# Kernel optimization log

Hardware: AMD Instinct MI355X
Metric: run time of the kernel (lower is better)

## Reference

```python
import jax, jax.numpy as jnp
import numpy as np

N_NODES = 65536
DEGREE = 16
N_EDGES = N_NODES * DEGREE
IN_CH = 128
HEADS = 4
OUT_CH = 16
NEG_SLOPE = 0.2


def setup_inputs() -> dict:
    key = jax.random.key(0)
    k1, k2, k3, k4, k5, k6 = jax.random.split(key, 6)
    csr_row_ptr = jnp.arange(N_NODES + 1, dtype=jnp.int64) * DEGREE
    csr_col_ind = jax.random.randint(k1, (N_EDGES,), 0, N_NODES, dtype=jnp.int64)
    sample_count = jnp.ones((N_NODES,), dtype=jnp.int64)
    x_neighboor = jax.random.normal(k2, (N_NODES, IN_CH), dtype=jnp.float32)
    x_target = jax.random.normal(k3, (N_NODES, IN_CH), dtype=jnp.float32)
    # xavier-ish init scales
    W = jax.random.normal(k4, (IN_CH, HEADS * OUT_CH), dtype=jnp.float32) * (2.0 / (IN_CH + HEADS * OUT_CH)) ** 0.5
    attn_l = jax.random.normal(k5, (HEADS, OUT_CH), dtype=jnp.float32) * 0.1
    attn_r = jax.random.normal(k6, (HEADS, OUT_CH), dtype=jnp.float32) * 0.1
    bias = jnp.zeros((HEADS * OUT_CH,), dtype=jnp.float32)
    return {"csr_row_ptr": csr_row_ptr, "csr_col_ind": csr_col_ind,
            "sample_count": sample_count, "x_neighboor": x_neighboor,
            "x_target": x_target, "W": W, "attn_l": attn_l,
            "attn_r": attn_r, "bias": bias}


def reference(csr_row_ptr, csr_col_ind, sample_count, x_neighboor, x_target, W, attn_l, attn_r, bias):
    N = csr_row_ptr.shape[0] - 1
    E = csr_col_ind.shape[0]
    H, C = attn_l.shape
    # linear projection: [Nn, in] @ [in, H*C] -> [Nn, H, C]
    feat = (x_neighboor @ W).reshape(-1, H, C)
    feat_target = feat[:N]
    el = jnp.sum(feat_target * attn_l[None], axis=-1)  # [N, H]
    er = jnp.sum(feat * attn_r[None], axis=-1)         # [Nn, H]
    # row id of each edge from CSR row pointers
    row_id = jnp.searchsorted(csr_row_ptr, jnp.arange(E), side='right') - 1  # [E]
    # spadd_gat: per-edge score = el[row] + er[col], then leaky relu
    w = el[row_id] + er[csr_col_ind]                   # [E, H]
    w = jnp.where(w >= 0, w, NEG_SLOPE * w)
    # segment (per-row) softmax over edges, numerically stable
    wmax = jax.lax.stop_gradient(jax.ops.segment_max(w, row_id, num_segments=N))
    ew = jnp.exp(w - wmax[row_id])
    denom = jax.ops.segment_sum(ew, row_id, num_segments=N)
    alpha = ew / denom[row_id]                         # [E, H]
    # weighted sparse aggregation (gspmm): y[r] = sum_e alpha[e] * feat[col[e]]
    y = jax.ops.segment_sum(alpha[:, :, None] * feat[csr_col_ind], row_id, num_segments=N)  # [N, H, C]
    y = y + bias.reshape(1, H, C)
    return y.reshape(N, H * C)
```

## Files before the change

kernel.cpp:

```cpp
#include <hip/hip_runtime.h>
#include <hip/hip_bf16.h>

#define IN_CH 128
#define HC 64
#define NEG_SLOPE 0.2f

typedef __attribute__((ext_vector_type(8))) short short8;
typedef __attribute__((ext_vector_type(4))) float floatx4;

__device__ __forceinline__ unsigned short f2bf_rne(float f) {
    unsigned int u = __float_as_uint(f);
    u += 0x7fffu + ((u >> 16) & 1u);
    return (unsigned short)(u >> 16);
}
__device__ __forceinline__ float bf2f(unsigned short u) {
    union { unsigned int i; float f; } v; v.i = ((unsigned int)u) << 16; return v.f;
}

__global__ __launch_bounds__(256, 4) void feat_gemm_kernel(
    const float* __restrict__ xf,
    const float* __restrict__ Wf,
    const float* __restrict__ attn_l,
    const float* __restrict__ attn_r,
    unsigned short* __restrict__ feat,
    float* __restrict__ el,
    float* __restrict__ er,
    int N)
{
    __shared__ unsigned short xb[64 * IN_CH];
    __shared__ unsigned short wb[IN_CH * HC];
    const int tid = threadIdx.x;
    const int row0 = blockIdx.x * 64;

    {
        const int row = tid >> 2;
        const int t   = row >> 4;
        const int mp  = row & 15;
        const int c   = tid & 3;
        const float4* src = (const float4*)(xf + (size_t)(row0 + row) * IN_CH + c * 32);
        #pragma unroll
        for (int i = 0; i < 8; ++i) {
            float4 v = src[i];
            const int q  = i >> 1;
            const int j0 = (i & 1) * 4;
            const int lane = q * 16 + mp;
            unsigned int p0 = (unsigned int)f2bf_rne(v.x) | ((unsigned int)f2bf_rne(v.y) << 16);
            unsigned int p1 = (unsigned int)f2bf_rne(v.z) | ((unsigned int)f2bf_rne(v.w) << 16);
            uint2 pk = make_uint2(p0, p1);
            *(uint2*)&xb[(((t * 4 + c) * 64 + lane) * 8) + j0] = pk;
        }
    }
    {
        const float4* W4 = (const float4*)Wf;
        #pragma unroll
        for (int i = 0; i < 8; ++i) {
            int fi = tid + 256 * i;
            float4 v = W4[fi];
            int k  = fi >> 4;
            int n0 = (fi & 15) * 4;
            int c  = k >> 5;
            int q  = (k & 31) >> 3;
            int j  = k & 7;
            int ct  = n0 >> 4;
            int np0 = n0 & 15;
            float e[4] = {v.x, v.y, v.z, v.w};
            #pragma unroll
            for (int t2 = 0; t2 < 4; ++t2) {
                int lane = q * 16 + (np0 + t2);
                wb[(((ct * 4 + c) * 64 + lane) * 8) + j] = f2bf_rne(e[t2]);
            }
        }
    }
    __syncthreads();

    const int w   = tid >> 6;
    const int lane = tid & 63;

    floatx4 acc[4];
    #pragma unroll
    for (int ct = 0; ct < 4; ++ct) acc[ct] = (floatx4){0.f, 0.f, 0.f, 0.f};

    #pragma unroll
    for (int c = 0; c < 4; ++c) {
        short8 afrag = *(const short8*)&xb[((w * 4 + c) * 64 + lane) * 8];
        #pragma unroll
        for (int ct = 0; ct < 4; ++ct) {
            short8 bfrag = *(const short8*)&wb[((ct * 4 + c) * 64 + lane) * 8];
            acc[ct] = __builtin_amdgcn_mfma_f32_16x16x32_bf16(afrag, bfrag, acc[ct], 0, 0, 0);
        }
    }

    const int q  = lane >> 4;
    const int np = lane & 15;
    float al[4], ar[4];
    #pragma unroll
    for (int h = 0; h < 4; ++h) { al[h] = attn_l[h * 16 + np]; ar[h] = attn_r[h * 16 + np]; }

    #pragma unroll
    for (int ct = 0; ct < 4; ++ct) {
        #pragma unroll
        for (int r = 0; r < 4; ++r) {
            int row = row0 + w * 16 + q * 4 + r;
            float v = acc[ct][r];
            feat[(size_t)row * HC + ct * 16 + np] = f2bf_rne(v);
            float pl = v * al[ct];
            float pr = v * ar[ct];
            #pragma unroll
            for (int o = 8; o >= 1; o >>= 1) {
                pl += __shfl_xor(pl, o, 16);
                pr += __shfl_xor(pr, o, 16);
            }
            if (np == 0) {
                el[row * 4 + ct] = pl;
                er[row * 4 + ct] = pr;
            }
        }
    }
}

__global__ __launch_bounds__(256) void gat_aggregate_kernel(
    const int* __restrict__ row_ptr32,
    const int* __restrict__ col_ind32,
    const unsigned short* __restrict__ feat,
    const float* __restrict__ el,
    const float* __restrict__ er,
    const float* __restrict__ bias,
    float* __restrict__ out,
    int N)
{
    const int lane = threadIdx.x & 63;
    const int node = blockIdx.x * 4 + (threadIdx.x >> 6);
    if (node >= N) return;

    const bool idx64 = (row_ptr32[1] != 16);
    int start, deg;
    if (idx64) {
        start = row_ptr32[2 * node];
        deg   = row_ptr32[2 * node + 2] - start;
    } else {
        start = row_ptr32[node];
        deg   = row_ptr32[node + 1] - start;
    }

    const int e = lane & 15;
    const int h = lane >> 4;
    int colv = 0;
    if (lane < 16 && lane < deg) {
        int ei = start + lane;
        colv = idx64 ? col_ind32[2 * ei] : col_ind32[ei];
    }
    int cole = __shfl(colv, e, 64);

    float w;
    if (e < deg) {
        float ww = el[node * 4 + h] + er[(size_t)cole * 4 + h];
        w = (ww >= 0.f) ? ww : NEG_SLOPE * ww;
    } else {
        w = -INFINITY;
    }
    float m = w;
    #pragma unroll
    for (int o = 8; o >= 1; o >>= 1) m = fmaxf(m, __shfl_xor(m, o, 16));
    float ew = (e < deg) ? __expf(w - m) : 0.f;
    float s = ew;
    #pragma unroll
    for (int o = 8; o >= 1; o >>= 1) s += __shfl_xor(s, o, 16);
    float alpha = (s > 0.f) ? (ew / s) : 0.f;

    float acc = 0.f;
    #pragma unroll
    for (int e2 = 0; e2 < 16; ++e2) {
        int c2 = __shfl(colv, e2, 64);
        float a = __shfl(alpha, (lane & 48) + e2, 64);
        acc += a * bf2f(feat[(size_t)c2 * HC + lane]);
    }
    acc += bias[lane];
    out[(size_t)node * HC + lane] = acc;
}

extern "C" void kernel_launch(void* const* d_in, const int* in_sizes, int n_in,
                              void* d_out, int out_size, void* d_ws, size_t ws_size,
                              hipStream_t stream) {
    const int* row_ptr      = (const int*)d_in[0];
    const int* col_ind      = (const int*)d_in[1];
    const float* x          = (const float*)d_in[3];
    const float* W          = (const float*)d_in[5];
    const float* attn_l     = (const float*)d_in[6];
    const float* attn_r     = (const float*)d_in[7];
    const float* bias       = (const float*)d_in[8];

    const int N = out_size / HC;

    unsigned short* feat = (unsigned short*)d_ws;
    float* el = (float*)((char*)d_ws + (size_t)N * HC * sizeof(unsigned short));
    float* er = el + (size_t)N * 4;

    feat_gemm_kernel<<<N / 64, 256, 0, stream>>>(x, W, attn_l, attn_r, feat, el, er, N);
    gat_aggregate_kernel<<<(N + 3) / 4, 256, 0, stream>>>(row_ptr, col_ind, feat, el, er, bias,
                                                          (float*)d_out, N);
}
```

Measured before the change: 150.9 us.

## Fold attention vectors into weights and prepack bf16 weights in a prep kernel

Adds a single-block prep kernel that converts W to a bf16 MFMA-ready layout once, and precomputes W·attn_l and W·attn_r so el/er come from one extra MFMA instead of shuffle reductions. The GEMM kernel now copies the prepacked weights into shared memory instead of converting fp32 W in every block. el and er are interleaved into one buffer so each node's scores sit together. The cost is an extra kernel launch and a slight precision change, since el/er are now computed from bf16-rounded folded weights.

```diff
diff --git a/kernel.cpp b/kernel.cpp
--- a/kernel.cpp
+++ b/kernel.cpp
@@ -17,21 +17,70 @@
     union { unsigned int i; float f; } v; v.i = ((unsigned int)u) << 16; return v.f;
 }
 
+__global__ void prep_kernel(const float* __restrict__ Wf,
+                            const float* __restrict__ attn_l,
+                            const float* __restrict__ attn_r,
+                            unsigned short* __restrict__ wb,
+                            unsigned short* __restrict__ wab)
+{
+    const int tid = threadIdx.x;
+    const float4* W4 = (const float4*)Wf;
+    #pragma unroll
+    for (int i = 0; i < 8; ++i) {
+        int fi = tid + 256 * i;
+        float4 v = W4[fi];
+        int k  = fi >> 4;
+        int n0 = (fi & 15) * 4;
+        int c = k >> 5, q = (k & 31) >> 3, j = k & 7;
+        int ct = n0 >> 4, np0 = n0 & 15;
+        float e[4] = {v.x, v.y, v.z, v.w};
+        #pragma unroll
+        for (int t2 = 0; t2 < 4; ++t2) {
+            int lane = q * 16 + np0 + t2;
+            wb[((ct * 4 + c) * 64 + lane) * 8 + j] = f2bf_rne(e[t2]);
+        }
+    }
+    if (tid < 128) {
+        int k = tid;
+        int c = k >> 5, q = (k & 31) >> 3, j = k & 7;
+        float wa[8];
+        #pragma unroll
+        for (int h = 0; h < 4; ++h) {
+            float sl = 0.f, sr = 0.f;
+            #pragma unroll
+            for (int cc = 0; cc < 16; ++cc) {
+                float wkc = Wf[k * HC + h * 16 + cc];
+                sl += wkc * attn_l[h * 16 + cc];
+                sr += wkc * attn_r[h * 16 + cc];
+            }
+            wa[h] = sl; wa[4 + h] = sr;
+        }
+        #pragma unroll
+        for (int n = 0; n < 16; ++n) {
+            int lane = q * 16 + n;
+            wab[(c * 64 + lane) * 8 + j] = (n < 8) ? f2bf_rne(wa[n]) : (unsigned short)0;
+        }
+    }
+}
+
 __global__ __launch_bounds__(256, 4) void feat_gemm_kernel(
     const float* __restrict__ xf,
-    const float* __restrict__ Wf,
-    const float* __restrict__ attn_l,
-    const float* __restrict__ attn_r,
+    const unsigned short* __restrict__ wbg,
     unsigned short* __restrict__ feat,
-    float* __restrict__ el,
-    float* __restrict__ er,
+    float* __restrict__ elr,
     int N)
 {
     __shared__ unsigned short xb[64 * IN_CH];
-    __shared__ unsigned short wb[IN_CH * HC];
+    __shared__ unsigned short lw[10240];
     const int tid = threadIdx.x;
     const int row0 = blockIdx.x * 64;
 
+    {
+        const uint4* src = (const uint4*)wbg;
+        uint4* dst = (uint4*)lw;
+        #pragma unroll
+        for (int i = 0; i < 5; ++i) dst[tid + 256 * i] = src[tid + 256 * i];
+    }
     {
         const int row = tid >> 2;
         const int t   = row >> 4;
@@ -46,74 +95,46 @@
             const int lane = q * 16 + mp;
             unsigned int p0 = (unsigned int)f2bf_rne(v.x) | ((unsigned int)f2bf_rne(v.y) << 16);
             unsigned int p1 = (unsigned int)f2bf_rne(v.z) | ((unsigned int)f2bf_rne(v.w) << 16);
-            uint2 pk = make_uint2(p0, p1);
-            *(uint2*)&xb[(((t * 4 + c) * 64 + lane) * 8) + j0] = pk;
-        }
-    }
-    {
-        const float4* W4 = (const float4*)Wf;
-        #pragma unroll
-        for (int i = 0; i < 8; ++i) {
-            int fi = tid + 256 * i;
-            float4 v = W4[fi];
-            int k  = fi >> 4;
-            int n0 = (fi & 15) * 4;
-            int c  = k >> 5;
-            int q  = (k & 31) >> 3;
-            int j  = k & 7;
-            int ct  = n0 >> 4;
-            int np0 = n0 & 15;
-            float e[4] = {v.x, v.y, v.z, v.w};
-            #pragma unroll
-            for (int t2 = 0; t2 < 4; ++t2) {
-                int lane = q * 16 + (np0 + t2);
-                wb[(((ct * 4 + c) * 64 + lane) * 8) + j] = f2bf_rne(e[t2]);
-            }
+            *(uint2*)&xb[(((t * 4 + c) * 64 + lane) * 8) + j0] = make_uint2(p0, p1);
         }
     }
     __syncthreads();
 
-    const int w   = tid >> 6;
+    const int w    = tid >> 6;
     const int lane = tid & 63;
 
-    floatx4 acc[4];
+    floatx4 acc[4], accA;
     #pragma unroll
     for (int ct = 0; ct < 4; ++ct) acc[ct] = (floatx4){0.f, 0.f, 0.f, 0.f};
+    accA = (floatx4){0.f, 0.f, 0.f, 0.f};
 
     #pragma unroll
     for (int c = 0; c < 4; ++c) {
         short8 afrag = *(const short8*)&xb[((w * 4 + c) * 64 + lane) * 8];
+        short8 wafrag = *(const short8*)&lw[8192 + (c * 64 + lane) * 8];
+        accA = __builtin_amdgcn_mfma_f32_16x16x32_bf16(afrag, wafrag, accA, 0, 0, 0);
         #pragma unroll
         for (int ct = 0; ct < 4; ++ct) {
-            short8 bfrag = *(const short8*)&wb[((ct * 4 + c) * 64 + lane) * 8];
+            short8 bfrag = *(const short8*)&lw[((ct * 4 + c) * 64 + lane) * 8];
             acc[ct] = __builtin_amdgcn_mfma_f32_16x16x32_bf16(afrag, bfrag, acc[ct], 0, 0, 0);
         }
     }
 
     const int q  = lane >> 4;
     const int np = lane & 15;
-    float al[4], ar[4];
-    #pragma unroll
-    for (int h = 0; h < 4; ++h) { al[h] = attn_l[h * 16 + np]; ar[h] = attn_r[h * 16 + np]; }
-
     #pragma unroll
     for (int ct = 0; ct < 4; ++ct) {
         #pragma unroll
         for (int r = 0; r < 4; ++r) {
             int row = row0 + w * 16 + q * 4 + r;
-            float v = acc[ct][r];
-            feat[(size_t)row * HC + ct * 16 + np] = f2bf_rne(v);
-            float pl = v * al[ct];
-            float pr = v * ar[ct];
-            #pragma unroll
-            for (int o = 8; o >= 1; o >>= 1) {
-                pl += __shfl_xor(pl, o, 16);
-                pr += __shfl_xor(pr, o, 16);
-            }
-            if (np == 0) {
-                el[row * 4 + ct] = pl;
-                er[row * 4 + ct] = pr;
-            }
+            feat[(size_t)row * HC + ct * 16 + np] = f2bf_rne(acc[ct][r]);
+        }
+    }
+    if (np < 8) {
+        #pragma unroll
+        for (int r = 0; r < 4; ++r) {
+            int row = row0 + w * 16 + q * 4 + r;
+            elr[(size_t)row * 8 + np] = accA[r];
         }
     }
 }
@@ -122,8 +143,7 @@
     const int* __restrict__ row_ptr32,
     const int* __restrict__ col_ind32,
     const unsigned short* __restrict__ feat,
-    const float* __restrict__ el,
-    const float* __restrict__ er,
+    const float* __restrict__ elr,
     const float* __restrict__ bias,
     float* __restrict__ out,
     int N)
@@ -153,7 +173,7 @@
 
     float w;
     if (e < deg) {
-        float ww = el[node * 4 + h] + er[(size_t)cole * 4 + h];
+        float ww = elr[(size_t)node * 8 + h] + elr[(size_t)cole * 8 + 4 + h];
         w = (ww >= 0.f) ? ww : NEG_SLOPE * ww;
     } else {
         w = -INFINITY;
@@ -192,10 +212,12 @@
     const int N = out_size / HC;
 
     unsigned short* feat = (unsigned short*)d_ws;
-    float* el = (float*)((char*)d_ws + (size_t)N * HC * sizeof(unsigned short));
-    float* er = el + (size_t)N * 4;
-
-    feat_gemm_kernel<<<N / 64, 256, 0, stream>>>(x, W, attn_l, attn_r, feat, el, er, N);
-    gat_aggregate_kernel<<<(N + 3) / 4, 256, 0, stream>>>(row_ptr, col_ind, feat, el, er, bias,
+    float* elr = (float*)((char*)d_ws + (size_t)N * HC * sizeof(unsigned short));
+    unsigned short* wb  = (unsigned short*)(elr + (size_t)N * 8);
+    unsigned short* wab = wb + 8192;
+
+    prep_kernel<<<1, 256, 0, stream>>>(W, attn_l, attn_r, wb, wab);
+    feat_gemm_kernel<<<N / 64, 256, 0, stream>>>(x, wb, feat, elr, N);
+    gat_aggregate_kernel<<<(N + 3) / 4, 256, 0, stream>>>(row_ptr, col_ind, feat, elr, bias,
                                                           (float*)d_out, N);
 }
```

Result: no change. 150.7 us (-0.1%).
